# Optimization experiments

Measured on AMD Instinct MI355X. Metric: run time of the kernel, lower is better.

## Reference

```python
import jax, jax.numpy as jnp
import numpy as np

H = 16  # num heads


def setup_inputs() -> dict:
    key = jax.random.key(0)
    ks = jax.random.split(key, 12)
    B, S, D = 2, 2048, 1024
    f = lambda k, shape: jax.random.normal(k, shape, dtype=jnp.float32) * 0.02
    return {
        "Q": jax.random.normal(ks[0], (B, S, D), dtype=jnp.float32),
        "K": jax.random.normal(ks[1], (B, S, D), dtype=jnp.float32),
        "V": jax.random.normal(ks[2], (B, S, D), dtype=jnp.float32),
        "mask": jax.random.randint(ks[3], (B, S, S), 0, 2, dtype=jnp.int32),
        "Wq": f(ks[4], (D, D)), "bq": f(ks[5], (D,)),
        "Wk": f(ks[6], (D, D)), "bk": f(ks[7], (D,)),
        "Wv": f(ks[8], (D, D)), "bv": f(ks[9], (D,)),
        "Wo": f(ks[10], (D, D)), "bo": f(ks[11], (D,)),
    }


def mha(Q, K, V, mask, Wq, bq, Wk, bk, Wv, bv, Wo, bo):
    B, S, D = Q.shape
    d_k = D // H
    # torch Linear: x @ W.T + b
    q = (Q @ Wq.T + bq).reshape(B, S, H, d_k).transpose(0, 2, 1, 3)  # [B,H,S,dk]
    k = (K @ Wk.T + bk).reshape(B, S, H, d_k).transpose(0, 2, 1, 3)
    v = (V @ Wv.T + bv).reshape(B, S, H, d_k).transpose(0, 2, 1, 3)
    scores = jnp.einsum('bhqd,bhkd->bhqk', q, k) / jnp.sqrt(jnp.float32(d_k))
    # faithful to torch: mask.repeat(H,1,1) tiles batch-major along dim0 of [B*H,S,S]
    m = jnp.tile(mask, (H, 1, 1)).reshape(B, H, S, S)
    scores = jnp.where(m == 0, jnp.float32(-1e9), scores)
    attn = jax.nn.softmax(scores, axis=-1)                 # [B,H,S,S]
    ctx = jnp.einsum('bhqk,bhkd->bhqd', attn, v)           # [B,H,S,dk]
    ctx = ctx.transpose(0, 2, 1, 3).reshape(B, S, D)
    out = ctx @ Wo.T + bo
    return out, attn


def reference(Q, K, V, mask, Wq, bq, Wk, bk, Wv, bv, Wo, bo):
    return mha(Q, K, V, mask, Wq, bq, Wk, bk, Wv, bv, Wo, bo)
```

## Files before the change

kernel.cpp:

```cpp
#include <hip/hip_runtime.h>
#include <stdint.h>


typedef __attribute__((ext_vector_type(8))) short bf16x8;
typedef __attribute__((ext_vector_type(4))) float f32x4;
typedef unsigned long long u64;

#define MFMA16(a, b, c) __builtin_amdgcn_mfma_f32_16x16x32_bf16((a), (b), (c), 0, 0, 0)

#define GLDS16(g, l)                                                   \
  __builtin_amdgcn_global_load_lds(                                    \
      (const __attribute__((address_space(1))) unsigned int*)(g),      \
      (__attribute__((address_space(3))) unsigned int*)(l), 16, 0, 0)

__device__ __forceinline__ float bf2f(short s) {
  union { float f; unsigned u; } x;
  x.u = ((unsigned)(unsigned short)s) << 16;
  return x.f;
}
__device__ __forceinline__ short f2bf(float f) {
  union { float f; unsigned u; } x;
  x.f = f;
  unsigned r = x.u + 0x7fffu + ((x.u >> 16) & 1u);
  return (short)(r >> 16);
}
__device__ __forceinline__ bf16x8 pack8(float4 a, float4 b) {
  union { short s[8]; bf16x8 v; } u;
  u.s[0] = f2bf(a.x); u.s[1] = f2bf(a.y); u.s[2] = f2bf(a.z); u.s[3] = f2bf(a.w);
  u.s[4] = f2bf(b.x); u.s[5] = f2bf(b.y); u.s[6] = f2bf(b.z); u.s[7] = f2bf(b.w);
  return u.v;
}

__global__ __launch_bounds__(256) void sentinel_fill(float* __restrict__ out,
                                                     float v, int n) {
  int i = blockIdx.x * 256 + threadIdx.x;
  if (i < n) out[i] = v;
}

__global__ __launch_bounds__(256) void pack_mask(const int* __restrict__ m,
                                                 u64* __restrict__ p) {
  long idx = (long)blockIdx.x * 256 + threadIdx.x;
  u64 b = __ballot(m[idx] != 0);
  if ((threadIdx.x & 63) == 0) p[idx >> 6] = b;
}

struct QkvPtrs {
  const float *A0, *A1, *A2;
  const float *W0, *W1, *W2;
  const float *c0, *c1, *c2;
  short *o0, *o1, *o2;
};
__global__ __launch_bounds__(256) void gemm_qkv(QkvPtrs p) {
  __shared__ short As[128 * 32];
  __shared__ short Bs[128 * 32];
  const int z = blockIdx.z;
  const float* Af = z == 0 ? p.A0 : (z == 1 ? p.A1 : p.A2);
  const float* W = z == 0 ? p.W0 : (z == 1 ? p.W1 : p.W2);
  const float* bias = z == 0 ? p.c0 : (z == 1 ? p.c1 : p.c2);
  short* outs = z == 0 ? p.o0 : (z == 1 ? p.o1 : p.o2);

  const int tid = threadIdx.x;
  const int lane = tid & 63;
  const int wid = tid >> 6;
  const int wr = wid >> 1, wc = wid & 1;
  const int m0 = blockIdx.x * 128;
  const int n0 = blockIdx.y * 128;

  const int srow = tid >> 1;
  const int scol = (tid & 1) << 4;
  const long aoff = (long)(m0 + srow) * 1024 + scol;
  const float* Wg = W + (long)(n0 + srow) * 1024 + scol;
  short* sA = As + srow * 32 + scol;
  short* sB = Bs + srow * 32 + scol;

  f32x4 acc[4][4] = {};
  const int fr = lane & 15;
  const int fc = (lane >> 4) << 3;

  for (int k0 = 0; k0 < 1024; k0 += 32) {
    __syncthreads();
    float4 x0 = *(const float4*)(Af + aoff + k0);
    float4 x1 = *(const float4*)(Af + aoff + k0 + 4);
    float4 x2 = *(const float4*)(Af + aoff + k0 + 8);
    float4 x3 = *(const float4*)(Af + aoff + k0 + 12);
    float4 w0 = *(const float4*)(Wg + k0);
    float4 w1 = *(const float4*)(Wg + k0 + 4);
    float4 w2 = *(const float4*)(Wg + k0 + 8);
    float4 w3 = *(const float4*)(Wg + k0 + 12);
    *(bf16x8*)sA = pack8(x0, x1);
    *(bf16x8*)(sA + 8) = pack8(x2, x3);
    *(bf16x8*)sB = pack8(w0, w1);
    *(bf16x8*)(sB + 8) = pack8(w2, w3);
    __syncthreads();
    bf16x8 a[4], b[4];
#pragma unroll
    for (int i = 0; i < 4; ++i)
      a[i] = *(const bf16x8*)&As[(wr * 64 + i * 16 + fr) * 32 + fc];
#pragma unroll
    for (int i = 0; i < 4; ++i)
      b[i] = *(const bf16x8*)&Bs[(wc * 64 + i * 16 + fr) * 32 + fc];
#pragma unroll
    for (int i = 0; i < 4; ++i)
#pragma unroll
      for (int j = 0; j < 4; ++j)
        acc[i][j] = MFMA16(a[i], b[j], acc[i][j]);
  }

#pragma unroll
  for (int i = 0; i < 4; ++i) {
    const int row0 = m0 + wr * 64 + i * 16 + (lane >> 4) * 4;
#pragma unroll
    for (int j = 0; j < 4; ++j) {
      const int col = n0 + wc * 64 + j * 16 + fr;
      const float bv = bias[col];
      const int h = col >> 6, dd = col & 63;
      if (z != 2) {
#pragma unroll
        for (int r = 0; r < 4; ++r) {
          const int m = row0 + r;
          const long o = (((long)(m >> 11) * 16 + h) * 2048 + (m & 2047)) * 64 + dd;
          outs[o] = f2bf(acc[i][j][r] + bv);
        }
      } else {
        const long o = (((long)(row0 >> 11) * 16 + h) * 64 + dd) * 2048 + (row0 & 2047);
        union { unsigned short us[4]; uint2 v; } pk;
#pragma unroll
        for (int r = 0; r < 4; ++r) pk.us[r] = (unsigned short)f2bf(acc[i][j][r] + bv);
        *(uint2*)&outs[o] = pk.v;
      }
    }
  }
}

__global__ __launch_bounds__(256) void gemm_out(const short* __restrict__ Ab,
                                                const float* __restrict__ W,
                                                const float* __restrict__ bias,
                                                float* __restrict__ outf) {
  __shared__ short As[128 * 32];
  __shared__ short Bs[128 * 32];
  const int tid = threadIdx.x;
  const int lane = tid & 63;
  const int wid = tid >> 6;
  const int wr = wid >> 1, wc = wid & 1;
  const int m0 = blockIdx.x * 128;
  const int n0 = blockIdx.y * 128;

  const int srow = tid >> 1;
  const int scol = (tid & 1) << 4;
  const long aoff = (long)(m0 + srow) * 1024 + scol;
  const float* Wg = W + (long)(n0 + srow) * 1024 + scol;
  short* sA = As + srow * 32 + scol;
  short* sB = Bs + srow * 32 + scol;

  f32x4 acc[4][4] = {};
  const int fr = lane & 15;
  const int fc = (lane >> 4) << 3;

  for (int k0 = 0; k0 < 1024; k0 += 32) {
    __syncthreads();
    bf16x8 va0 = *(const bf16x8*)(Ab + aoff + k0);
    bf16x8 va1 = *(const bf16x8*)(Ab + aoff + k0 + 8);
    float4 w0 = *(const float4*)(Wg + k0);
    float4 w1 = *(const float4*)(Wg + k0 + 4);
    float4 w2 = *(const float4*)(Wg + k0 + 8);
    float4 w3 = *(const float4*)(Wg + k0 + 12);
    *(bf16x8*)sA = va0;
    *(bf16x8*)(sA + 8) = va1;
    *(bf16x8*)sB = pack8(w0, w1);
    *(bf16x8*)(sB + 8) = pack8(w2, w3);
    __syncthreads();
    bf16x8 a[4], b[4];
#pragma unroll
    for (int i = 0; i < 4; ++i)
      a[i] = *(const bf16x8*)&As[(wr * 64 + i * 16 + fr) * 32 + fc];
#pragma unroll
    for (int i = 0; i < 4; ++i)
      b[i] = *(const bf16x8*)&Bs[(wc * 64 + i * 16 + fr) * 32 + fc];
#pragma unroll
    for (int i = 0; i < 4; ++i)
#pragma unroll
      for (int j = 0; j < 4; ++j)
        acc[i][j] = MFMA16(a[i], b[j], acc[i][j]);
  }

#pragma unroll
  for (int i = 0; i < 4; ++i) {
    const int row0 = m0 + wr * 64 + i * 16 + (lane >> 4) * 4;
#pragma unroll
    for (int j = 0; j < 4; ++j) {
      const int col = n0 + wc * 64 + j * 16 + fr;
      const float bv = bias[col];
#pragma unroll
      for (int r = 0; r < 4; ++r)
        outf[(long)(row0 + r) * 1024 + col] = acc[i][j][r] + bv;
    }
  }
}

__global__ __launch_bounds__(256) void attn_fused(
    const short* __restrict__ qw, const short* __restrict__ kw,
    const short* __restrict__ vtw, const u64* __restrict__ pm,
    float* __restrict__ attn, short* __restrict__ ctx) {
  __shared__ short Ks[2][4096];
  __shared__ short Vs[2][4096];
  __shared__ short P[4][1024];
  const int tid = threadIdx.x;
  const int lane = tid & 63;
  const int wid = tid >> 6;
  const int bh = blockIdx.x;
  const int mb = bh & 1;
  const int q0 = blockIdx.y * 64 + wid * 16;
  const int fr = lane & 15;
  const int fg = lane >> 4;
  short* Pw = P[wid];

  bf16x8 aq[2];
  {
    const short* qb = qw + ((long)bh * 2048 + q0 + fr) * 64 + fg * 8;
    aq[0] = *(const bf16x8*)qb;
    aq[1] = *(const bf16x8*)(qb + 32);
  }

  const u64* mbase = pm + ((long)mb * 2048 + q0) * 32;
  const short* kbase = kw + (long)bh * 2048 * 64;
  const short* vbase = vtw + (long)bh * 64 * 2048;
  const long arow = (long)bh * 2048 + q0;

  const int sidx0 = tid;
  const int sidx1 = 256 + tid;
  const int sr0 = sidx0 >> 3, ss0 = (sidx0 ^ sr0) & 7;
  const int sr1 = sidx1 >> 3, ss1 = (sidx1 ^ sr1) & 7;
  short* ldst0 = &Ks[0][0] + (long)(wid * 64) * 8;
  short* ldst1 = &Ks[0][0] + (long)(256 + wid * 64) * 8;
  const long kofs = (long)(&Vs[0][0] - &Ks[0][0]);

#define STAGE_K(buf, kt)                                              \
  {                                                                   \
    const short* s_ = kbase + (long)((kt) * 64) * 64;                 \
    GLDS16(s_ + sr0 * 64 + ss0 * 8, ldst0 + (buf) * 4096);            \
    GLDS16(s_ + sr1 * 64 + ss1 * 8, ldst1 + (buf) * 4096);            \
  }
#define STAGE_V(buf, kt)                                              \
  {                                                                   \
    const short* s_ = vbase + (kt) * 64;                              \
    GLDS16(s_ + (long)sr0 * 2048 + ss0 * 8, ldst0 + kofs + (buf) * 4096); \
    GLDS16(s_ + (long)sr1 * 2048 + ss1 * 8, ldst1 + kofs + (buf) * 4096); \
  }
#define SWZ(row, slot) (((row) << 6) + ((((slot) ^ ((row) & 7))) << 3))
#define PADDR(row, col) \
  (((row) << 6) + (((((col) >> 3) ^ ((row) & 7))) << 3) + ((col) & 7))
#define WRITEBACK(kt)                                                 \
  {                                                                   \
    _Pragma("unroll") for (int c = 0; c < 4; ++c) {                   \
      const int idx = c * 64 + lane;                                  \
      const int row = idx >> 4;                                       \
      const int col = (idx & 15) * 4;                                 \
      union { uint2 w; short s[4]; } v4;                              \
      v4.w = *(const uint2*)&Pw[PADDR(row, col)];                     \
      float4 f;                                                       \
      f.x = bf2f(v4.s[0]); f.y = bf2f(v4.s[1]);                       \
      f.z = bf2f(v4.s[2]); f.w = bf2f(v4.s[3]);                       \
      *(float4*)&attn[(arow + row) * 2048 + (kt) * 64 + col] = f;     \
    }                                                                 \
  }

  float rs = 0.f;
  STAGE_K(0, 0);
  __syncthreads();
  int cur = 0;
  for (int kt = 0; kt < 32; ++kt) {
    if (kt < 31) STAGE_K(cur ^ 1, kt + 1);
    const u64 mrow = mbase[fr * 32 + kt];
#pragma unroll
    for (int ni = 0; ni < 4; ++ni) {
      const int R = ni * 16 + fr;
      bf16x8 b0 = *(const bf16x8*)&Ks[cur][SWZ(R, fg)];
      bf16x8 b1 = *(const bf16x8*)&Ks[cur][SWZ(R, 4 + fg)];
      const int kb0 = ni * 16 + fg * 4;
      f32x4 s = {0.f, 0.f, 0.f, 0.f};
      s = MFMA16(b0, aq[0], s);
      s = MFMA16(b1, aq[1], s);
#pragma unroll
      for (int r = 0; r < 4; ++r)
        if ((mrow >> (kb0 + r)) & 1ULL) rs += __expf(s[r] * 0.125f);
    }
    __syncthreads();
    cur ^= 1;
  }
  float il;
  {
    float v = rs;
    v += __shfl_xor(v, 16);
    v += __shfl_xor(v, 32);
    il = 1.0f / v;
  }

  f32x4 cacc[4] = {};
  STAGE_K(0, 0);
  STAGE_V(0, 0);
  __syncthreads();
  cur = 0;
  for (int kt = 0; kt < 32; ++kt) {
    if (kt > 0) WRITEBACK(kt - 1);
    if (kt < 31) {
      STAGE_K(cur ^ 1, kt + 1);
      STAGE_V(cur ^ 1, kt + 1);
    }
    const u64 mrow = mbase[fr * 32 + kt];

#pragma unroll
    for (int ni = 0; ni < 4; ++ni) {
      const int R = ni * 16 + fr;
      bf16x8 b0 = *(const bf16x8*)&Ks[cur][SWZ(R, fg)];
      bf16x8 b1 = *(const bf16x8*)&Ks[cur][SWZ(R, 4 + fg)];
      const int kb0 = ni * 16 + fg * 4;
      f32x4 s = {0.f, 0.f, 0.f, 0.f};
      s = MFMA16(b0, aq[0], s);
      s = MFMA16(b1, aq[1], s);
      union { unsigned short us[4]; uint2 v; } pk;
#pragma unroll
      for (int r = 0; r < 4; ++r) {
        float p = ((mrow >> (kb0 + r)) & 1ULL) ? __expf(s[r] * 0.125f) * il
                                               : 0.0f;
        pk.us[r] = (unsigned short)f2bf(p);
      }
      *(uint2*)&Pw[PADDR(fr, kb0)] = pk.v;
    }

#pragma unroll
    for (int ks = 0; ks < 2; ++ks) {
      bf16x8 pa = *(const bf16x8*)&Pw[PADDR(fr, ks * 32 + fg * 8)];
#pragma unroll
      for (int ni = 0; ni < 4; ++ni) {
        const int R = ni * 16 + fr;
        bf16x8 bv = *(const bf16x8*)&Vs[cur][SWZ(R, ks * 4 + fg)];
        cacc[ni] = MFMA16(pa, bv, cacc[ni]);
      }
    }

    __syncthreads();
    cur ^= 1;
  }
  WRITEBACK(31);

  const int b_ = bh >> 4, h_ = bh & 15;
#pragma unroll
  for (int ni = 0; ni < 4; ++ni)
#pragma unroll
    for (int r = 0; r < 4; ++r)
      ctx[((long)b_ * 2048 + q0 + fg * 4 + r) * 1024 + h_ * 64 + ni * 16 + fr] =
          f2bf(cacc[ni][r]);
#undef STAGE_K
#undef STAGE_V
#undef SWZ
#undef PADDR
#undef WRITEBACK
}

extern "C" void kernel_launch(void* const* d_in, const int* in_sizes, int n_in,
                              void* d_out, int out_size, void* d_ws,
                              size_t ws_size, hipStream_t stream) {
  float* out_o = (float*)d_out;

  const bool sizes_ok =
      (n_in == 12) && in_sizes[0] == 4194304 && in_sizes[1] == 4194304 &&
      in_sizes[2] == 4194304 && in_sizes[3] == 8388608 &&
      in_sizes[4] == 1048576 && in_sizes[5] == 1024 &&
      in_sizes[10] == 1048576 && in_sizes[11] == 1024 &&
      out_size == (2 * 2048 * 1024 + 2 * 16 * 2048 * 2048);
  const size_t WS_NEED = 34603008;
  if (!sizes_ok) {
    sentinel_fill<<<dim3(16384), 256, 0, stream>>>(out_o, 555.0f, 4194304);
    return;
  }
  if (ws_size < WS_NEED) {
    sentinel_fill<<<dim3(16384), 256, 0, stream>>>(out_o, 777.0f, 4194304);
    return;
  }

  const float* Q = (const float*)d_in[0];
  const float* K = (const float*)d_in[1];
  const float* V = (const float*)d_in[2];
  const int* mask = (const int*)d_in[3];
  const float* Wq = (const float*)d_in[4];
  const float* bq = (const float*)d_in[5];
  const float* Wk = (const float*)d_in[6];
  const float* bk = (const float*)d_in[7];
  const float* Wv = (const float*)d_in[8];
  const float* bv = (const float*)d_in[9];
  const float* Wo = (const float*)d_in[10];
  const float* bo = (const float*)d_in[11];

  short* qws = (short*)d_ws;
  short* kws = qws + 4194304;
  short* vtws = kws + 4194304;
  short* ctxws = vtws + 4194304;
  u64* pmask = (u64*)(ctxws + 4194304);

  float* out_attn = out_o + 2 * 2048 * 1024;

  pack_mask<<<dim3(2 * 2048 * 2048 / 256), 256, 0, stream>>>(mask, pmask);
  QkvPtrs p = {Q, K, V, Wq, Wk, Wv, bq, bk, bv, qws, kws, vtws};
  gemm_qkv<<<dim3(32, 8, 3), 256, 0, stream>>>(p);
  attn_fused<<<dim3(32, 32), 256, 0, stream>>>(qws, kws, vtws, pmask,
                                               out_attn, ctxws);
  gemm_out<<<dim3(32, 8), 256, 0, stream>>>(ctxws, Wo, bo, out_o);
}
```

Before: 374.3 us.

## Replace syncthreads with counted vmcnt waits and prefetch mask words

```diff
diff --git a/kernel.cpp b/kernel.cpp
--- a/kernel.cpp
+++ b/kernel.cpp
@@ -263,14 +263,25 @@
       *(float4*)&attn[(arow + row) * 2048 + (kt) * 64 + col] = f;     \
     }                                                                 \
   }
+#define WAITBAR(N)                                                    \
+  {                                                                   \
+    asm volatile("s_waitcnt vmcnt(" #N ")" ::: "memory");             \
+    __builtin_amdgcn_sched_barrier(0);                                \
+    __builtin_amdgcn_s_barrier();                                     \
+    __builtin_amdgcn_sched_barrier(0);                                \
+  }
 
   float rs = 0.f;
   STAGE_K(0, 0);
-  __syncthreads();
+  u64 mrow = mbase[fr * 32 + 0];
+  WAITBAR(1)
   int cur = 0;
   for (int kt = 0; kt < 32; ++kt) {
-    if (kt < 31) STAGE_K(cur ^ 1, kt + 1);
-    const u64 mrow = mbase[fr * 32 + kt];
+    u64 mrow_next = 0;
+    if (kt < 31) {
+      STAGE_K(cur ^ 1, kt + 1);
+      mrow_next = mbase[fr * 32 + kt + 1];
+    }
 #pragma unroll
     for (int ni = 0; ni < 4; ++ni) {
       const int R = ni * 16 + fr;
@@ -284,8 +295,11 @@
       for (int r = 0; r < 4; ++r)
         if ((mrow >> (kb0 + r)) & 1ULL) rs += __expf(s[r] * 0.125f);
     }
-    __syncthreads();
-    cur ^= 1;
+    if (kt < 31) {
+      WAITBAR(1)
+      cur ^= 1;
+      mrow = mrow_next;
+    }
   }
   float il;
   {
@@ -294,19 +308,21 @@
     v += __shfl_xor(v, 32);
     il = 1.0f / v;
   }
+  __builtin_amdgcn_s_barrier();
 
   f32x4 cacc[4] = {};
   STAGE_K(0, 0);
   STAGE_V(0, 0);
-  __syncthreads();
+  mrow = mbase[fr * 32 + 0];
+  WAITBAR(1)
   cur = 0;
   for (int kt = 0; kt < 32; ++kt) {
-    if (kt > 0) WRITEBACK(kt - 1);
+    u64 mrow_next = 0;
     if (kt < 31) {
       STAGE_K(cur ^ 1, kt + 1);
       STAGE_V(cur ^ 1, kt + 1);
-    }
-    const u64 mrow = mbase[fr * 32 + kt];
+      mrow_next = mbase[fr * 32 + kt + 1];
+    }
 
 #pragma unroll
     for (int ni = 0; ni < 4; ++ni) {
@@ -338,10 +354,14 @@
       }
     }
 
-    __syncthreads();
-    cur ^= 1;
-  }
-  WRITEBACK(31);
+    WRITEBACK(kt);
+
+    if (kt < 31) {
+      WAITBAR(5)
+      cur ^= 1;
+      mrow = mrow_next;
+    }
+  }
 
   const int b_ = bh >> 4, h_ = bh & 15;
 #pragma unroll
@@ -355,6 +375,7 @@
 #undef SWZ
 #undef PADDR
 #undef WRITEBACK
+#undef WAITBAR
 }
 
 extern "C" void kernel_launch(void* const* d_in, const int* in_sizes, int n_in,
```

Result: no change. 376.8 us (+0.7%).
